# Kernel optimization log

Measured on AMD Instinct MI355X. Metric: run time of the kernel, lower is better.

Reference implementation:

```python
import jax, jax.numpy as jnp
import numpy as np

N_NODES = 100000
N_EDGES = 3200000
N_GRAPHS = 1000

def setup_inputs() -> dict:
    key = jax.random.key(0)
    ks = jax.random.split(key, 8)
    x = jax.random.normal(ks[0], (N_NODES, 4), dtype=jnp.float32)
    edge_index = jax.random.randint(ks[1], (2, N_EDGES), 0, N_NODES, dtype=jnp.int64)
    batch = jnp.sort(jax.random.randint(ks[2], (N_NODES,), 0, N_GRAPHS, dtype=jnp.int64))
    def glorot(k, shape):
        lim = np.sqrt(6.0 / (shape[0] + shape[1]))
        return jax.random.uniform(k, shape, jnp.float32, -lim, lim)
    return {
        'x': x, 'edge_index': edge_index, 'batch': batch,
        'W1': glorot(ks[3], (4, 16)),  'b1': jnp.zeros((16,), jnp.float32),
        'W2': glorot(ks[4], (16, 16)), 'b2': jnp.zeros((16,), jnp.float32),
        'W3': glorot(ks[5], (16, 16)), 'b3': jnp.zeros((16,), jnp.float32),
        'lin_w': glorot(ks[6], (16, 1)), 'lin_b': jnp.zeros((1,), jnp.float32),
    }

def _gcn_norm(edge_index, num_nodes):
    # PyG GCNConv default: add self-loops, symmetric normalization
    loop = jnp.arange(num_nodes, dtype=edge_index.dtype)
    row = jnp.concatenate([edge_index[0], loop])  # source
    col = jnp.concatenate([edge_index[1], loop])  # target
    ones = jnp.ones(row.shape[0], dtype=jnp.float32)
    deg = jax.ops.segment_sum(ones, col, num_segments=num_nodes)
    dinv = jnp.where(deg > 0, jax.lax.rsqrt(deg), 0.0)
    norm = dinv[row] * dinv[col]  # [E+N]
    return row, col, norm

def _gcn_conv(x, row, col, norm, W, b, num_nodes):
    h = x @ W                                   # small GEMM first (fewer msg bytes)
    msg = h[row] * norm[:, None]                # gather + scale
    out = jax.ops.segment_sum(msg, col, num_segments=num_nodes)  # scatter-add
    return out + b

def reference(x, edge_index, batch, W1, b1, W2, b2, W3, b3, lin_w, lin_b):
    n = x.shape[0]
    row, col, norm = _gcn_norm(edge_index, n)
    h = _gcn_conv(x, row, col, norm, W1, b1, n)
    h = _gcn_conv(h, row, col, norm, W2, b2, n)
    h = _gcn_conv(h, row, col, norm, W3, b3, n)
    # global_mean_pool
    sums = jax.ops.segment_sum(h, batch, num_segments=N_GRAPHS)
    cnt = jax.ops.segment_sum(jnp.ones((n,), jnp.float32), batch, num_segments=N_GRAPHS)
    pooled = sums / jnp.maximum(cnt, 1.0)[:, None]
    # dropout p=0.5 is identity in eval mode
    logits = pooled @ lin_w + lin_b
    return jax.nn.sigmoid(logits)
```

## Files before the change

kernel.cpp:

```cpp
#include <hip/hip_runtime.h>
#include <math.h>


#define SHIFT      8
#define BSZ        256
#define NB_SCAT    256
#define SCAN_CHUNK 2048
#define PNODES     1024
#define ROWMASK    0x1FFFFu

__global__ void coeffs_kernel(const float* __restrict__ W1, const float* __restrict__ b1,
                              const float* __restrict__ W2, const float* __restrict__ b2,
                              const float* __restrict__ W3, const float* __restrict__ b3,
                              const float* __restrict__ lin_w, const float* __restrict__ lin_b,
                              float* __restrict__ coeff) {
    if (threadIdx.x == 0 && blockIdx.x == 0) {
        float w3l[16], w2l[16];
        for (int i = 0; i < 16; ++i) {
            float s = 0.f;
            for (int j = 0; j < 16; ++j) s += W3[i * 16 + j] * lin_w[j];
            w3l[i] = s;
        }
        for (int i = 0; i < 16; ++i) {
            float s = 0.f;
            for (int j = 0; j < 16; ++j) s += W2[i * 16 + j] * w3l[j];
            w2l[i] = s;
        }
        for (int i = 0; i < 4; ++i) {
            float s = 0.f;
            for (int j = 0; j < 16; ++j) s += W1[i * 16 + j] * w2l[j];
            coeff[i] = s;
        }
        float s2 = 0.f, s1 = 0.f, s0 = 0.f;
        for (int j = 0; j < 16; ++j) {
            s2 += b1[j] * w2l[j];
            s1 += b2[j] * w3l[j];
            s0 += b3[j] * lin_w[j];
        }
        coeff[4] = s2; coeff[5] = s1; coeff[6] = s0; coeff[7] = lin_b[0];
    }
}

__global__ void zero_pool_kernel(float* __restrict__ sums, float* __restrict__ cnt, int ngraphs) {
    int i = blockIdx.x * blockDim.x + threadIdx.x;
    if (i < ngraphs) { sums[i] = 0.f; cnt[i] = 0.f; }
}

__global__ void hist_kernel(const int* __restrict__ col, int E, int tile, int nbuck,
                            unsigned* __restrict__ M) {
    extern __shared__ unsigned h[];
    for (int i = threadIdx.x; i < nbuck; i += blockDim.x) h[i] = 0;
    __syncthreads();
    int b = blockIdx.x;
    int s = b * tile, e = min(s + tile, E);
    if (s < e) {
        int nq = (e - s) >> 2;
        const int4* c4 = (const int4*)(col + s);
        for (int q = threadIdx.x; q < nq; q += blockDim.x) {
            int4 c = c4[q];
            atomicAdd(&h[((unsigned)c.x) >> SHIFT], 1u);
            atomicAdd(&h[((unsigned)c.y) >> SHIFT], 1u);
            atomicAdd(&h[((unsigned)c.z) >> SHIFT], 1u);
            atomicAdd(&h[((unsigned)c.w) >> SHIFT], 1u);
        }
        for (int k = s + (nq << 2) + threadIdx.x; k < e; k += blockDim.x)
            atomicAdd(&h[((unsigned)col[k]) >> SHIFT], 1u);
    }
    __syncthreads();
    for (int i = threadIdx.x; i < nbuck; i += blockDim.x)
        M[(size_t)i * NB_SCAT + b] = h[i];
}

__global__ void scan1_kernel(const unsigned* __restrict__ M, unsigned* __restrict__ part,
                             int total, int chunk) {
    __shared__ unsigned sdata[256];
    int b = blockIdx.x;
    int s = b * chunk, e = min(s + chunk, total);
    unsigned sum = 0;
    for (int k = s + threadIdx.x; k < e; k += blockDim.x) sum += M[k];
    sdata[threadIdx.x] = sum;
    __syncthreads();
    for (int off = 128; off > 0; off >>= 1) {
        if (threadIdx.x < off) sdata[threadIdx.x] += sdata[threadIdx.x + off];
        __syncthreads();
    }
    if (threadIdx.x == 0) part[b] = sdata[0];
}

__global__ void scan2_kernel(unsigned* __restrict__ part, int np) {
    if (threadIdx.x == 0 && blockIdx.x == 0) {
        unsigned run = 0;
        for (int i = 0; i < np; ++i) { unsigned v = part[i]; part[i] = run; run += v; }
    }
}

__global__ void scan3_kernel(unsigned* __restrict__ M, const unsigned* __restrict__ part,
                             int total, int chunk) {
    __shared__ unsigned ts[256];
    int b = blockIdx.x;
    int s = b * chunk;
    const int per = SCAN_CHUNK / 256;
    unsigned v[per];
    unsigned sum = 0;
    int base = s + threadIdx.x * per;
    for (int j = 0; j < per; ++j) {
        unsigned x = (base + j < total) ? M[base + j] : 0u;
        v[j] = sum; sum += x;
    }
    ts[threadIdx.x] = sum;
    __syncthreads();
    for (int off = 1; off < 256; off <<= 1) {
        unsigned t = (threadIdx.x >= (unsigned)off) ? ts[threadIdx.x - off] : 0u;
        __syncthreads();
        ts[threadIdx.x] += t;
        __syncthreads();
    }
    unsigned texcl = (threadIdx.x == 0) ? 0u : ts[threadIdx.x - 1];
    unsigned pb = part[b];
    for (int j = 0; j < per; ++j)
        if (base + j < total) M[base + j] = pb + texcl + v[j];
}

__global__ void scatter_kernel(const int* __restrict__ row, const int* __restrict__ col,
                               int E, int tile, int nbuck, const unsigned* __restrict__ M,
                               unsigned* __restrict__ out) {
    extern __shared__ unsigned base[];
    int b = blockIdx.x;
    for (int i = threadIdx.x; i < nbuck; i += blockDim.x)
        base[i] = M[(size_t)i * NB_SCAT + b];
    __syncthreads();
    int s = b * tile, e = min(s + tile, E);
    if (s < e) {
        int nq = (e - s) >> 2;
        const int4* r4 = (const int4*)(row + s);
        const int4* c4 = (const int4*)(col + s);
        for (int q = threadIdx.x; q < nq; q += blockDim.x) {
            int4 r = r4[q];
            int4 c = c4[q];
            unsigned p0 = atomicAdd(&base[((unsigned)c.x) >> SHIFT], 1u);
            unsigned p1 = atomicAdd(&base[((unsigned)c.y) >> SHIFT], 1u);
            unsigned p2 = atomicAdd(&base[((unsigned)c.z) >> SHIFT], 1u);
            unsigned p3 = atomicAdd(&base[((unsigned)c.w) >> SHIFT], 1u);
            out[p0] = (unsigned)r.x | (((unsigned)c.x & (BSZ - 1)) << 17);
            out[p1] = (unsigned)r.y | (((unsigned)c.y & (BSZ - 1)) << 17);
            out[p2] = (unsigned)r.z | (((unsigned)c.z & (BSZ - 1)) << 17);
            out[p3] = (unsigned)r.w | (((unsigned)c.w & (BSZ - 1)) << 17);
        }
        for (int k = s + (nq << 2) + threadIdx.x; k < e; k += blockDim.x) {
            unsigned c = (unsigned)col[k];
            unsigned pos = atomicAdd(&base[c >> SHIFT], 1u);
            out[pos] = (unsigned)row[k] | ((c & (BSZ - 1)) << 17);
        }
    }
}

__global__ void deg0_kernel(const unsigned* __restrict__ buck, const unsigned* __restrict__ M,
                            int nbuck, int E, const float* __restrict__ x,
                            const float* __restrict__ coeff, float* __restrict__ dinv,
                            float* __restrict__ g, int n) {
    __shared__ float acc[BSZ];
    int b = blockIdx.x;
    acc[threadIdx.x] = 0.f;
    __syncthreads();
    unsigned s = M[(size_t)b * NB_SCAT];
    unsigned e = (b + 1 < nbuck) ? M[(size_t)(b + 1) * NB_SCAT] : (unsigned)E;
    unsigned sa = (s + 3u) & ~3u;
    if (sa > e) sa = e;
    if (s + threadIdx.x < sa)
        atomicAdd(&acc[buck[s + threadIdx.x] >> 17], 1.0f);
    unsigned nq = (e - sa) >> 2;
    const uint4* bq = (const uint4*)(buck + sa);
    for (unsigned q = threadIdx.x; q < nq; q += blockDim.x) {
        uint4 w = bq[q];
        atomicAdd(&acc[w.x >> 17], 1.0f);
        atomicAdd(&acc[w.y >> 17], 1.0f);
        atomicAdd(&acc[w.z >> 17], 1.0f);
        atomicAdd(&acc[w.w >> 17], 1.0f);
    }
    for (unsigned k = sa + (nq << 2) + threadIdx.x; k < e; k += blockDim.x)
        atomicAdd(&acc[buck[k] >> 17], 1.0f);
    __syncthreads();
    int node = b * BSZ + threadIdx.x;
    if (node < n) {
        float d = rsqrtf(acc[threadIdx.x] + 1.0f);
        dinv[node] = d;
        float4 xv = ((const float4*)x)[node];
        float t0 = xv.x * coeff[0] + xv.y * coeff[1] + xv.z * coeff[2] + xv.w * coeff[3];
        g[node] = d * t0;
    }
}

__global__ void gather_kernel(const unsigned* __restrict__ buck, const unsigned* __restrict__ M,
                              int nbuck, int E, const float* __restrict__ dinv,
                              const float* __restrict__ gin, float* __restrict__ gout,
                              const float* __restrict__ coeff, int sidx, int n, int lastPass) {
    __shared__ float acc[BSZ];
    int b = blockIdx.x;
    acc[threadIdx.x] = 0.f;
    __syncthreads();
    unsigned s = M[(size_t)b * NB_SCAT];
    unsigned e = (b + 1 < nbuck) ? M[(size_t)(b + 1) * NB_SCAT] : (unsigned)E;
    unsigned sa = (s + 3u) & ~3u;
    if (sa > e) sa = e;
    if (s + threadIdx.x < sa) {
        unsigned w = buck[s + threadIdx.x];
        atomicAdd(&acc[w >> 17], gin[w & ROWMASK]);
    }
    unsigned nq = (e - sa) >> 2;
    const uint4* bq = (const uint4*)(buck + sa);
    for (unsigned q = threadIdx.x; q < nq; q += blockDim.x) {
        uint4 w = bq[q];
        float a0 = gin[w.x & ROWMASK];
        float a1 = gin[w.y & ROWMASK];
        float a2 = gin[w.z & ROWMASK];
        float a3 = gin[w.w & ROWMASK];
        atomicAdd(&acc[w.x >> 17], a0);
        atomicAdd(&acc[w.y >> 17], a1);
        atomicAdd(&acc[w.z >> 17], a2);
        atomicAdd(&acc[w.w >> 17], a3);
    }
    for (unsigned k = sa + (nq << 2) + threadIdx.x; k < e; k += blockDim.x) {
        unsigned w = buck[k];
        atomicAdd(&acc[w >> 17], gin[w & ROWMASK]);
    }
    __syncthreads();
    int node = b * BSZ + threadIdx.x;
    if (node < n) {
        float d = dinv[node];
        float t = d * (acc[threadIdx.x] + gin[node]) + coeff[sidx];
        gout[node] = lastPass ? t : d * t;
    }
}

__global__ void pool_kernel(const float* __restrict__ t3, const int* __restrict__ batch,
                            float* __restrict__ sums, float* __restrict__ cnt, int n) {
    __shared__ float ls[1024];
    __shared__ float lc[1024];
    int s = blockIdx.x * PNODES, e = min(s + PNODES, n);
    if (s >= e) return;
    int bFirst = batch[s];
    int bLast  = batch[e - 1];
    int range = bLast - bFirst + 1;
    if (range <= 1024) {
        for (int i = threadIdx.x; i < range; i += blockDim.x) { ls[i] = 0.f; lc[i] = 0.f; }
        __syncthreads();
        for (int k = s + threadIdx.x; k < e; k += blockDim.x) {
            int bb = batch[k] - bFirst;
            atomicAdd(&ls[bb], t3[k]);
            atomicAdd(&lc[bb], 1.0f);
        }
        __syncthreads();
        for (int i = threadIdx.x; i < range; i += blockDim.x) {
            if (lc[i] != 0.f) {
                atomicAdd(&sums[bFirst + i], ls[i]);
                atomicAdd(&cnt[bFirst + i], lc[i]);
            }
        }
    } else {
        for (int k = s + threadIdx.x; k < e; k += blockDim.x) {
            atomicAdd(&sums[batch[k]], t3[k]);
            atomicAdd(&cnt[batch[k]], 1.0f);
        }
    }
}

__global__ void final_kernel(const float* __restrict__ sums, const float* __restrict__ cnt,
                             const float* __restrict__ coeff, float* __restrict__ out,
                             int ngraphs) {
    int i = blockIdx.x * blockDim.x + threadIdx.x;
    if (i < ngraphs) {
        float m = sums[i] / fmaxf(cnt[i], 1.0f) + coeff[7];
        out[i] = 1.0f / (1.0f + expf(-m));
    }
}

__global__ void fb_init_kernel(float* __restrict__ deg, float* __restrict__ sums,
                               float* __restrict__ cnt, int n, int ngraphs) {
    int i = blockIdx.x * blockDim.x + threadIdx.x;
    int stride = gridDim.x * blockDim.x;
    for (int k = i; k < n; k += stride) deg[k] = 1.0f;
    for (int k = i; k < ngraphs; k += stride) { sums[k] = 0.f; cnt[k] = 0.f; }
}
__global__ void fb_deg_kernel(const int* __restrict__ col, float* __restrict__ deg, int E) {
    int i = blockIdx.x * blockDim.x + threadIdx.x;
    int stride = gridDim.x * blockDim.x;
    for (int k = i; k < E; k += stride) atomicAdd(&deg[col[k]], 1.0f);
}
__global__ void fb_node0_kernel(const float* __restrict__ x, const float* __restrict__ coeff,
                                float* __restrict__ deg_dinv, float* __restrict__ g,
                                float* __restrict__ acc, int n) {
    int i = blockIdx.x * blockDim.x + threadIdx.x;
    int stride = gridDim.x * blockDim.x;
    for (int k = i; k < n; k += stride) {
        float d = rsqrtf(deg_dinv[k]);
        deg_dinv[k] = d;
        float4 xv = ((const float4*)x)[k];
        float t0 = xv.x * coeff[0] + xv.y * coeff[1] + xv.z * coeff[2] + xv.w * coeff[3];
        g[k] = d * t0;
        acc[k] = 0.f;
    }
}
__global__ void fb_edge_kernel(const int* __restrict__ ei, const float* __restrict__ g,
                               float* __restrict__ acc, int E) {
    int i = blockIdx.x * blockDim.x + threadIdx.x;
    int stride = gridDim.x * blockDim.x;
    for (int k = i; k < E; k += stride) atomicAdd(&acc[ei[E + k]], g[ei[k]]);
}
__global__ void fb_node_kernel(const float* __restrict__ dinv, float* __restrict__ g,
                               float* __restrict__ acc, const float* __restrict__ coeff,
                               int sidx, int n) {
    int i = blockIdx.x * blockDim.x + threadIdx.x;
    int stride = gridDim.x * blockDim.x;
    for (int k = i; k < n; k += stride) {
        float d = dinv[k];
        float t = d * (acc[k] + g[k]) + coeff[sidx];
        g[k] = d * t;
        acc[k] = 0.f;
    }
}
__global__ void fb_pool_kernel(const float* __restrict__ dinv, const float* __restrict__ g,
                               const float* __restrict__ acc, const float* __restrict__ coeff,
                               const int* __restrict__ batch, float* __restrict__ sums,
                               float* __restrict__ cnt, int n) {
    int i = blockIdx.x * blockDim.x + threadIdx.x;
    int stride = gridDim.x * blockDim.x;
    for (int k = i; k < n; k += stride) {
        float d = dinv[k];
        float t3 = d * (acc[k] + g[k]) + coeff[6];
        int b = batch[k];
        atomicAdd(&sums[b], t3);
        atomicAdd(&cnt[b], 1.0f);
    }
}

extern "C" void kernel_launch(void* const* d_in, const int* in_sizes, int n_in,
                              void* d_out, int out_size, void* d_ws, size_t ws_size,
                              hipStream_t stream) {
    const float* x     = (const float*)d_in[0];
    const int*   ei    = (const int*)d_in[1];
    const int*   batch = (const int*)d_in[2];
    const float* W1    = (const float*)d_in[3];
    const float* b1    = (const float*)d_in[4];
    const float* W2    = (const float*)d_in[5];
    const float* b2    = (const float*)d_in[6];
    const float* W3    = (const float*)d_in[7];
    const float* b3    = (const float*)d_in[8];
    const float* lin_w = (const float*)d_in[9];
    const float* lin_b = (const float*)d_in[10];

    const int n       = in_sizes[0] / 4;
    const int E       = in_sizes[1] / 2;
    const int ngraphs = out_size;

    const int nbuck = (n + BSZ - 1) / BSZ;
    const int B = 256;

    size_t npad = ((size_t)n + 255) & ~(size_t)255;
    size_t gpad = ((size_t)ngraphs + 255) & ~(size_t)255;
    size_t mlen = (size_t)nbuck * NB_SCAT;
    int total   = (int)mlen;
    int nchunks = (total + SCAN_CHUNK - 1) / SCAN_CHUNK;

    size_t need = (256 + mlen + 1024 + (size_t)E + 3 * npad + 2 * gpad) * 4;

    float* ws   = (float*)d_ws;
    float* coeff = ws;
    unsigned* M    = (unsigned*)(coeff + 256);
    unsigned* part = M + mlen;
    unsigned* buck = part + 1024;
    float* dinv  = (float*)(buck + E);
    float* gA    = dinv + npad;
    float* gB    = gA + npad;
    float* sums  = gB + npad;
    float* cnt   = sums + gpad;

    coeffs_kernel<<<1, 64, 0, stream>>>(W1, b1, W2, b2, W3, b3, lin_w, lin_b, coeff);

    if (ws_size < need) {
        float* deg = (float*)(ws + 256);
        float* g   = deg + npad;
        float* acc = g + npad;
        float* fsums = acc + npad;
        float* fcnt  = fsums + gpad;
        int nodeBlocks = (n + B - 1) / B;
        int edgeBlocks = (E + B - 1) / B;
        fb_init_kernel<<<nodeBlocks, B, 0, stream>>>(deg, fsums, fcnt, n, ngraphs);
        fb_deg_kernel<<<edgeBlocks, B, 0, stream>>>(ei + E, deg, E);
        fb_node0_kernel<<<nodeBlocks, B, 0, stream>>>(x, coeff, deg, g, acc, n);
        fb_edge_kernel<<<edgeBlocks, B, 0, stream>>>(ei, g, acc, E);
        fb_node_kernel<<<nodeBlocks, B, 0, stream>>>(deg, g, acc, coeff, 4, n);
        fb_edge_kernel<<<edgeBlocks, B, 0, stream>>>(ei, g, acc, E);
        fb_node_kernel<<<nodeBlocks, B, 0, stream>>>(deg, g, acc, coeff, 5, n);
        fb_edge_kernel<<<edgeBlocks, B, 0, stream>>>(ei, g, acc, E);
        fb_pool_kernel<<<nodeBlocks, B, 0, stream>>>(deg, g, acc, coeff, batch, fsums, fcnt, n);
        final_kernel<<<(ngraphs + B - 1) / B, B, 0, stream>>>(fsums, fcnt, coeff, (float*)d_out, ngraphs);
        return;
    }

    int tile = (((E + NB_SCAT - 1) / NB_SCAT) + 3) & ~3;
    size_t ldsHist = (size_t)nbuck * sizeof(unsigned);

    zero_pool_kernel<<<(ngraphs + B - 1) / B, B, 0, stream>>>(sums, cnt, ngraphs);

    hist_kernel<<<NB_SCAT, B, ldsHist, stream>>>(ei + E, E, tile, nbuck, M);
    scan1_kernel<<<nchunks, B, 0, stream>>>(M, part, total, SCAN_CHUNK);
    scan2_kernel<<<1, 64, 0, stream>>>(part, nchunks);
    scan3_kernel<<<nchunks, B, 0, stream>>>(M, part, total, SCAN_CHUNK);
    scatter_kernel<<<NB_SCAT, B, ldsHist, stream>>>(ei, ei + E, E, tile, nbuck, M, buck);

    deg0_kernel<<<nbuck, B, 0, stream>>>(buck, M, nbuck, E, x, coeff, dinv, gA, n);

    gather_kernel<<<nbuck, B, 0, stream>>>(buck, M, nbuck, E, dinv, gA, gB, coeff, 4, n, 0);
    gather_kernel<<<nbuck, B, 0, stream>>>(buck, M, nbuck, E, dinv, gB, gA, coeff, 5, n, 0);
    gather_kernel<<<nbuck, B, 0, stream>>>(buck, M, nbuck, E, dinv, gA, gB, coeff, 6, n, 1);

    pool_kernel<<<(n + PNODES - 1) / PNODES, B, 0, stream>>>(gB, batch, sums, cnt, n);

    final_kernel<<<(ngraphs + B - 1) / B, B, 0, stream>>>(sums, cnt, coeff, (float*)d_out, ngraphs);
}
```

Measured before the change: 157.8 us.

## Split per-bucket edge aggregation into segments with separate node finalize pass

```diff
diff --git a/kernel.cpp b/kernel.cpp
--- a/kernel.cpp
+++ b/kernel.cpp
@@ -8,13 +8,17 @@
 #define SCAN_CHUNK 2048
 #define PNODES     1024
 #define ROWMASK    0x1FFFFu
+#define SEG        8
+#define SEGSH      3
 
 __global__ void coeffs_kernel(const float* __restrict__ W1, const float* __restrict__ b1,
                               const float* __restrict__ W2, const float* __restrict__ b2,
                               const float* __restrict__ W3, const float* __restrict__ b3,
                               const float* __restrict__ lin_w, const float* __restrict__ lin_b,
-                              float* __restrict__ coeff) {
-    if (threadIdx.x == 0 && blockIdx.x == 0) {
+                              float* __restrict__ coeff,
+                              float* __restrict__ sums, float* __restrict__ cnt, int ngraphs) {
+    for (int i = threadIdx.x; i < ngraphs; i += blockDim.x) { sums[i] = 0.f; cnt[i] = 0.f; }
+    if (threadIdx.x == 0) {
         float w3l[16], w2l[16];
         for (int i = 0; i < 16; ++i) {
             float s = 0.f;
@@ -39,11 +43,6 @@
         }
         coeff[4] = s2; coeff[5] = s1; coeff[6] = s0; coeff[7] = lin_b[0];
     }
-}
-
-__global__ void zero_pool_kernel(float* __restrict__ sums, float* __restrict__ cnt, int ngraphs) {
-    int i = blockIdx.x * blockDim.x + threadIdx.x;
-    if (i < ngraphs) { sums[i] = 0.f; cnt[i] = 0.f; }
 }
 
 __global__ void hist_kernel(const int* __restrict__ col, int E, int tile, int nbuck,
@@ -154,21 +153,23 @@
     }
 }
 
-__global__ void deg0_kernel(const unsigned* __restrict__ buck, const unsigned* __restrict__ M,
-                            int nbuck, int E, const float* __restrict__ x,
-                            const float* __restrict__ coeff, float* __restrict__ dinv,
-                            float* __restrict__ g, int n) {
+__global__ void degseg_kernel(const unsigned* __restrict__ buck, const unsigned* __restrict__ M,
+                              int nbuck, int E, float* __restrict__ partial) {
     __shared__ float acc[BSZ];
-    int b = blockIdx.x;
+    int b = blockIdx.x >> SEGSH;
+    int sg = blockIdx.x & (SEG - 1);
     acc[threadIdx.x] = 0.f;
     __syncthreads();
-    unsigned s = M[(size_t)b * NB_SCAT];
-    unsigned e = (b + 1 < nbuck) ? M[(size_t)(b + 1) * NB_SCAT] : (unsigned)E;
-    unsigned sa = (s + 3u) & ~3u;
-    if (sa > e) sa = e;
-    if (s + threadIdx.x < sa)
-        atomicAdd(&acc[buck[s + threadIdx.x] >> 17], 1.0f);
-    unsigned nq = (e - sa) >> 2;
+    unsigned start = M[(size_t)b * NB_SCAT];
+    unsigned end = (b + 1 < nbuck) ? M[(size_t)(b + 1) * NB_SCAT] : (unsigned)E;
+    unsigned len = end - start;
+    unsigned s0 = start + (unsigned)(((unsigned long long)len * sg) >> SEGSH);
+    unsigned s1 = start + (unsigned)(((unsigned long long)len * (sg + 1)) >> SEGSH);
+    unsigned sa = (s0 + 3u) & ~3u;
+    if (sa > s1) sa = s1;
+    if (s0 + threadIdx.x < sa)
+        atomicAdd(&acc[buck[s0 + threadIdx.x] >> 17], 1.0f);
+    unsigned nq = (s1 - sa) >> 2;
     const uint4* bq = (const uint4*)(buck + sa);
     for (unsigned q = threadIdx.x; q < nq; q += blockDim.x) {
         uint4 w = bq[q];
@@ -177,36 +178,48 @@
         atomicAdd(&acc[w.z >> 17], 1.0f);
         atomicAdd(&acc[w.w >> 17], 1.0f);
     }
-    for (unsigned k = sa + (nq << 2) + threadIdx.x; k < e; k += blockDim.x)
+    for (unsigned k = sa + (nq << 2) + threadIdx.x; k < s1; k += blockDim.x)
         atomicAdd(&acc[buck[k] >> 17], 1.0f);
     __syncthreads();
-    int node = b * BSZ + threadIdx.x;
-    if (node < n) {
-        float d = rsqrtf(acc[threadIdx.x] + 1.0f);
-        dinv[node] = d;
-        float4 xv = ((const float4*)x)[node];
-        float t0 = xv.x * coeff[0] + xv.y * coeff[1] + xv.z * coeff[2] + xv.w * coeff[3];
-        g[node] = d * t0;
-    }
-}
-
-__global__ void gather_kernel(const unsigned* __restrict__ buck, const unsigned* __restrict__ M,
-                              int nbuck, int E, const float* __restrict__ dinv,
-                              const float* __restrict__ gin, float* __restrict__ gout,
-                              const float* __restrict__ coeff, int sidx, int n, int lastPass) {
+    partial[((size_t)sg * nbuck + b) * BSZ + threadIdx.x] = acc[threadIdx.x];
+}
+
+__global__ void node0_kernel(const float* __restrict__ partial, int nbuck,
+                             const float* __restrict__ x, const float* __restrict__ coeff,
+                             float* __restrict__ dinv, float* __restrict__ g, int n) {
+    int node = blockIdx.x * blockDim.x + threadIdx.x;
+    if (node >= n) return;
+    size_t slot = (size_t)blockIdx.x * BSZ + threadIdx.x;
+    float deg = 1.0f;
+    for (int sg = 0; sg < SEG; ++sg)
+        deg += partial[(size_t)sg * nbuck * BSZ + slot];
+    float d = rsqrtf(deg);
+    dinv[node] = d;
+    float4 xv = ((const float4*)x)[node];
+    float t0 = xv.x * coeff[0] + xv.y * coeff[1] + xv.z * coeff[2] + xv.w * coeff[3];
+    g[node] = d * t0;
+}
+
+__global__ void gatherseg_kernel(const unsigned* __restrict__ buck, const unsigned* __restrict__ M,
+                                 int nbuck, int E, const float* __restrict__ gin,
+                                 float* __restrict__ partial) {
     __shared__ float acc[BSZ];
-    int b = blockIdx.x;
+    int b = blockIdx.x >> SEGSH;
+    int sg = blockIdx.x & (SEG - 1);
     acc[threadIdx.x] = 0.f;
     __syncthreads();
-    unsigned s = M[(size_t)b * NB_SCAT];
-    unsigned e = (b + 1 < nbuck) ? M[(size_t)(b + 1) * NB_SCAT] : (unsigned)E;
-    unsigned sa = (s + 3u) & ~3u;
-    if (sa > e) sa = e;
-    if (s + threadIdx.x < sa) {
-        unsigned w = buck[s + threadIdx.x];
+    unsigned start = M[(size_t)b * NB_SCAT];
+    unsigned end = (b + 1 < nbuck) ? M[(size_t)(b + 1) * NB_SCAT] : (unsigned)E;
+    unsigned len = end - start;
+    unsigned s0 = start + (unsigned)(((unsigned long long)len * sg) >> SEGSH);
+    unsigned s1 = start + (unsigned)(((unsigned long long)len * (sg + 1)) >> SEGSH);
+    unsigned sa = (s0 + 3u) & ~3u;
+    if (sa > s1) sa = s1;
+    if (s0 + threadIdx.x < sa) {
+        unsigned w = buck[s0 + threadIdx.x];
         atomicAdd(&acc[w >> 17], gin[w & ROWMASK]);
     }
-    unsigned nq = (e - sa) >> 2;
+    unsigned nq = (s1 - sa) >> 2;
     const uint4* bq = (const uint4*)(buck + sa);
     for (unsigned q = threadIdx.x; q < nq; q += blockDim.x) {
         uint4 w = bq[q];
@@ -219,17 +232,27 @@
         atomicAdd(&acc[w.z >> 17], a2);
         atomicAdd(&acc[w.w >> 17], a3);
     }
-    for (unsigned k = sa + (nq << 2) + threadIdx.x; k < e; k += blockDim.x) {
+    for (unsigned k = sa + (nq << 2) + threadIdx.x; k < s1; k += blockDim.x) {
         unsigned w = buck[k];
         atomicAdd(&acc[w >> 17], gin[w & ROWMASK]);
     }
     __syncthreads();
-    int node = b * BSZ + threadIdx.x;
-    if (node < n) {
-        float d = dinv[node];
-        float t = d * (acc[threadIdx.x] + gin[node]) + coeff[sidx];
-        gout[node] = lastPass ? t : d * t;
-    }
+    partial[((size_t)sg * nbuck + b) * BSZ + threadIdx.x] = acc[threadIdx.x];
+}
+
+__global__ void nodefin_kernel(const float* __restrict__ partial, int nbuck,
+                               const float* __restrict__ dinv, const float* __restrict__ gin,
+                               float* __restrict__ gout, const float* __restrict__ coeff,
+                               int sidx, int n, int lastPass) {
+    int node = blockIdx.x * blockDim.x + threadIdx.x;
+    if (node >= n) return;
+    size_t slot = (size_t)blockIdx.x * BSZ + threadIdx.x;
+    float a = 0.f;
+    for (int sg = 0; sg < SEG; ++sg)
+        a += partial[(size_t)sg * nbuck * BSZ + slot];
+    float d = dinv[node];
+    float t = d * (a + gin[node]) + coeff[sidx];
+    gout[node] = lastPass ? t : d * t;
 }
 
 __global__ void pool_kernel(const float* __restrict__ t3, const int* __restrict__ batch,
@@ -358,49 +381,54 @@
     size_t npad = ((size_t)n + 255) & ~(size_t)255;
     size_t gpad = ((size_t)ngraphs + 255) & ~(size_t)255;
     size_t mlen = (size_t)nbuck * NB_SCAT;
+    size_t plen = (size_t)SEG * nbuck * BSZ;
     int total   = (int)mlen;
     int nchunks = (total + SCAN_CHUNK - 1) / SCAN_CHUNK;
 
-    size_t need = (256 + mlen + 1024 + (size_t)E + 3 * npad + 2 * gpad) * 4;
+    size_t need = (256 + mlen + 1024 + (size_t)E + plen + 3 * npad + 2 * gpad) * 4;
 
     float* ws   = (float*)d_ws;
     float* coeff = ws;
     unsigned* M    = (unsigned*)(coeff + 256);
     unsigned* part = M + mlen;
     unsigned* buck = part + 1024;
-    float* dinv  = (float*)(buck + E);
+    float* partial = (float*)(buck + E);
+    float* dinv  = partial + plen;
     float* gA    = dinv + npad;
     float* gB    = gA + npad;
     float* sums  = gB + npad;
     float* cnt   = sums + gpad;
 
-    coeffs_kernel<<<1, 64, 0, stream>>>(W1, b1, W2, b2, W3, b3, lin_w, lin_b, coeff);
-
     if (ws_size < need) {
-        float* deg = (float*)(ws + 256);
+        float* fcoeff = ws;
+        float* deg = fcoeff + 256;
         float* g   = deg + npad;
         float* acc = g + npad;
         float* fsums = acc + npad;
         float* fcnt  = fsums + gpad;
         int nodeBlocks = (n + B - 1) / B;
         int edgeBlocks = (E + B - 1) / B;
+        coeffs_kernel<<<1, 64, 0, stream>>>(W1, b1, W2, b2, W3, b3, lin_w, lin_b, fcoeff,
+                                            fsums, fcnt, ngraphs);
         fb_init_kernel<<<nodeBlocks, B, 0, stream>>>(deg, fsums, fcnt, n, ngraphs);
         fb_deg_kernel<<<edgeBlocks, B, 0, stream>>>(ei + E, deg, E);
-        fb_node0_kernel<<<nodeBlocks, B, 0, stream>>>(x, coeff, deg, g, acc, n);
+        fb_node0_kernel<<<nodeBlocks, B, 0, stream>>>(x, fcoeff, deg, g, acc, n);
         fb_edge_kernel<<<edgeBlocks, B, 0, stream>>>(ei, g, acc, E);
-        fb_node_kernel<<<nodeBlocks, B, 0, stream>>>(deg, g, acc, coeff, 4, n);
+        fb_node_kernel<<<nodeBlocks, B, 0, stream>>>(deg, g, acc, fcoeff, 4, n);
         fb_edge_kernel<<<edgeBlocks, B, 0, stream>>>(ei, g, acc, E);
-        fb_node_kernel<<<nodeBlocks, B, 0, stream>>>(deg, g, acc, coeff, 5, n);
+        fb_node_kernel<<<nodeBlocks, B, 0, stream>>>(deg, g, acc, fcoeff, 5, n);
         fb_edge_kernel<<<edgeBlocks, B, 0, stream>>>(ei, g, acc, E);
-        fb_pool_kernel<<<nodeBlocks, B, 0, stream>>>(deg, g, acc, coeff, batch, fsums, fcnt, n);
-        final_kernel<<<(ngraphs + B - 1) / B, B, 0, stream>>>(fsums, fcnt, coeff, (float*)d_out, ngraphs);
+        fb_pool_kernel<<<nodeBlocks, B, 0, stream>>>(deg, g, acc, fcoeff, batch, fsums, fcnt, n);
+        final_kernel<<<(ngraphs + B - 1) / B, B, 0, stream>>>(fsums, fcnt, fcoeff, (float*)d_out, ngraphs);
         return;
     }
 
     int tile = (((E + NB_SCAT - 1) / NB_SCAT) + 3) & ~3;
     size_t ldsHist = (size_t)nbuck * sizeof(unsigned);
-
-    zero_pool_kernel<<<(ngraphs + B - 1) / B, B, 0, stream>>>(sums, cnt, ngraphs);
+    int segBlocks = nbuck << SEGSH;
+
+    coeffs_kernel<<<1, B, 0, stream>>>(W1, b1, W2, b2, W3, b3, lin_w, lin_b, coeff,
+                                       sums, cnt, ngraphs);
 
     hist_kernel<<<NB_SCAT, B, ldsHist, stream>>>(ei + E, E, tile, nbuck, M);
     scan1_kernel<<<nchunks, B, 0, stream>>>(M, part, total, SCAN_CHUNK);
@@ -408,11 +436,15 @@
     scan3_kernel<<<nchunks, B, 0, stream>>>(M, part, total, SCAN_CHUNK);
     scatter_kernel<<<NB_SCAT, B, ldsHist, stream>>>(ei, ei + E, E, tile, nbuck, M, buck);
 
-    deg0_kernel<<<nbuck, B, 0, stream>>>(buck, M, nbuck, E, x, coeff, dinv, gA, n);
-
-    gather_kernel<<<nbuck, B, 0, stream>>>(buck, M, nbuck, E, dinv, gA, gB, coeff, 4, n, 0);
-    gather_kernel<<<nbuck, B, 0, stream>>>(buck, M, nbuck, E, dinv, gB, gA, coeff, 5, n, 0);
-    gather_kernel<<<nbuck, B, 0, stream>>>(buck, M, nbuck, E, dinv, gA, gB, coeff, 6, n, 1);
+    degseg_kernel<<<segBlocks, B, 0, stream>>>(buck, M, nbuck, E, partial);
+    node0_kernel<<<nbuck, B, 0, stream>>>(partial, nbuck, x, coeff, dinv, gA, n);
+
+    gatherseg_kernel<<<segBlocks, B, 0, stream>>>(buck, M, nbuck, E, gA, partial);
+    nodefin_kernel<<<nbuck, B, 0, stream>>>(partial, nbuck, dinv, gA, gB, coeff, 4, n, 0);
+    gatherseg_kernel<<<segBlocks, B, 0, stream>>>(buck, M, nbuck, E, gB, partial);
+    nodefin_kernel<<<nbuck, B, 0, stream>>>(partial, nbuck, dinv, gB, gA, coeff, 5, n, 0);
+    gatherseg_kernel<<<segBlocks, B, 0, stream>>>(buck, M, nbuck, E, gA, partial);
+    nodefin_kernel<<<nbuck, B, 0, stream>>>(partial, nbuck, dinv, gA, gB, coeff, 6, n, 1);
 
     pool_kernel<<<(n + PNODES - 1) / PNODES, B, 0, stream>>>(gB, batch, sums, cnt, n);
 
```

New measurement: 157.8 us. Within noise of the previous version (+0.0%).
